# Optimization experiments

Hardware: AMD Instinct MI355X
Metric: run time of the kernel (lower is better)

The kernel has to match this reference:

```python
import jax, jax.numpy as jnp
import numpy as np

N = 1_000_000   # mesh points
D_IN = 5        # scalar invariants
H = 128         # hidden width
L = 5           # hidden layers
NB = 10         # tensor bases

# t0 generator basis rows (flattened 3x3 deviatoric diag tensors)
T01 = np.array([-1/3, 0, 0, 0, 1/6, 0, 0, 0, 1/6], dtype=np.float32)
T02 = np.array([1/6, 0, 0, 0, -1/3, 0, 0, 0, 1/6], dtype=np.float32)
T03 = np.array([1/6, 0, 0, 0, 1/6, 0, 0, 0, -1/3], dtype=np.float32)


def _linear_params(k, fan_in, fan_out):
    # xavier_uniform_ with gain=1.0, bias filled with 0.01 (as in init_w_and_b)
    limit = float(np.sqrt(6.0 / (fan_in + fan_out)))
    W = jax.random.uniform(k, (fan_in, fan_out), jnp.float32, -limit, limit)
    b = jnp.full((fan_out,), 0.01, jnp.float32)
    return W, b


def setup_inputs() -> dict:
    key = jax.random.key(0)
    ks = jax.random.split(key, 16)
    x = jax.random.normal(ks[0], (N, D_IN), jnp.float32)
    tb = jax.random.normal(ks[1], (N, NB, 9), jnp.float32)
    inp = {"x": x, "tb": tb}
    dims = [D_IN] + [H] * L
    for i in range(L):
        W, b = _linear_params(ks[2 + i], dims[i], dims[i + 1])
        inp[f"W{i+1}"] = W
        inp[f"b{i+1}"] = b
    inp["Wc"], inp["bc"] = _linear_params(ks[2 + L], H, NB)
    inp["Wg1"], inp["bg1"] = _linear_params(ks[3 + L], H, 1)
    inp["Wg2"], inp["bg2"] = _linear_params(ks[4 + L], H, 1)
    inp["Wg3"], inp["bg3"] = _linear_params(ks[5 + L], H, 1)
    return inp


def reference(x, tb, W1, b1, W2, b2, W3, b3, W4, b4, W5, b5,
              Wc, bc, Wg1, bg1, Wg2, bg2, Wg3, bg3):
    h = x
    for W, b in ((W1, b1), (W2, b2), (W3, b3), (W4, b4), (W5, b5)):
        h = jax.nn.relu(h @ W + b)          # [N, H]
    coeffs = h @ Wc + bc                     # [N, NB]
    g1 = h @ Wg1 + bg1                       # [N, 1]
    g2 = h @ Wg2 + bg2
    g3 = h @ Wg3 + bg3
    t0 = g1 * jnp.asarray(T01) + g2 * jnp.asarray(T02) + g3 * jnp.asarray(T03)  # [N, 9]
    # batched tensor-basis contraction replacing the per-point double loop
    bij = t0 + jnp.einsum('nt,ntc->nc', coeffs, tb)  # [N, 9]
    return bij
```

## Files before the change

kernel.cpp:

```cpp
#include <hip/hip_runtime.h>
#include <stdint.h>


#define NPTS   1000000
#define TPB    512
#define NBLKS  256
#define PTILE  512
#define NT     ((NPTS + PTILE - 1) / PTILE)

typedef uint32_t u32;
typedef __attribute__((ext_vector_type(4)))  u32   u32x4;
typedef __attribute__((ext_vector_type(8)))  short s16x8;
typedef __attribute__((ext_vector_type(16))) float f32x16;
typedef __attribute__((ext_vector_type(4), aligned(4))) float f32x4u;

#define WS_L(l)   ((l)*65536)
#define WS_TAIL   262144
#define WS_W1     (262144 + 8192)
#define WS_BIAS   (262144 + 12288)

#define LDS_BUF0   0
#define LDS_BUF1   65536
#define LDS_HEADS  131072
#define LDS_W1     (131072 + 8192)
#define LDS_BIAS   (131072 + 12288)
#define LDS_TOTAL  147456

#define MFMA(a,b,c) __builtin_amdgcn_mfma_f32_32x32x16_bf16((a),(b),(c),0,0,0)
#define BC16(v)     __builtin_bit_cast(s16x8, (v))

__device__ __forceinline__ u32 cvtpk(float lo, float hi) {
    u32 r;
    asm("v_cvt_pk_bf16_f32 %0, %1, %2" : "=v"(r) : "v"(lo), "v"(hi));
    return r;
}
__device__ __forceinline__ float lo2f(u32 p){ return __builtin_bit_cast(float, p << 16); }
__device__ __forceinline__ float hi2f(u32 p){ return __builtin_bit_cast(float, p & 0xffff0000u); }
__device__ __forceinline__ uint16_t f2bf(float f) {
    u32 u = __builtin_bit_cast(u32, f);
    return (uint16_t)((u + 0x7fffu + ((u >> 16) & 1u)) >> 16);
}
__device__ __forceinline__ float b2f(uint16_t h){ return __builtin_bit_cast(float, (u32)h << 16); }

__device__ __forceinline__ void stageN(const char* g, char* l, int tid, int nbytes) {
    const int w = tid >> 6, ln = tid & 63;
    const char* gp = g + w*1024 + ln*16;
    char* lp = l + w*1024;
    #pragma unroll
    for (int i = 0; i < 8; ++i) {
        if (i*8192 >= nbytes) break;
        __builtin_amdgcn_global_load_lds(
            (const __attribute__((address_space(1))) uint32_t*)(gp + i*8192),
            (__attribute__((address_space(3))) uint32_t*)(lp + i*8192), 16, 0, 0);
    }
}

extern "C" __global__ void __launch_bounds__(256)
tbnn_prep(const float* __restrict__ W1, const float* __restrict__ b1,
          const float* __restrict__ W2, const float* __restrict__ b2,
          const float* __restrict__ W3, const float* __restrict__ b3,
          const float* __restrict__ W4, const float* __restrict__ b4,
          const float* __restrict__ W5, const float* __restrict__ b5,
          const float* __restrict__ Wc, const float* __restrict__ bc,
          const float* __restrict__ Wg1,const float* __restrict__ bg1,
          const float* __restrict__ Wg2,const float* __restrict__ bg2,
          const float* __restrict__ Wg3,const float* __restrict__ bg3,
          char* __restrict__ ws)
{
    int idx = blockIdx.x*256 + threadIdx.x;
    if (idx < 65536) {
        int l = idx >> 14, r = idx & 16383, ifc = r >> 7, of = r & 127;
        const float* Wt = (l==0)?W2:(l==1)?W3:(l==2)?W4:W5;
        float w = Wt[ifc*128 + of];
        uint16_t hb = f2bf(w);
        uint16_t lb = f2bf(w - b2f(hb));
        char* row = ws + WS_L(l) + of*512;
        int o = (2*ifc) ^ ((of&15)<<4);
        *(uint16_t*)(row + o)       = hb;
        *(uint16_t*)(row + 256 + o) = lb;
    } else if (idx < 65536 + 2048) {
        int j = idx - 65536, of = j >> 7, ifc = j & 127;
        float v = 0.f;
        if      (of < 10)  v = Wc[ifc*10 + of];
        else if (of == 10) v = Wg1[ifc];
        else if (of == 11) v = Wg2[ifc];
        else if (of == 12) v = Wg3[ifc];
        uint16_t hb = f2bf(v);
        uint16_t lb = f2bf(v - b2f(hb));
        char* row = ws + WS_TAIL + of*512;
        int o = (2*ifc) ^ ((of&15)<<4);
        *(uint16_t*)(row + o)       = hb;
        *(uint16_t*)(row + 256 + o) = lb;
    } else if (idx < 65536 + 2048 + 128) {
        int of = idx - (65536 + 2048);
        uint16_t* dst = (uint16_t*)(ws + WS_W1 + of*32);
        #pragma unroll
        for (int s = 0; s < 5; ++s) {
            float w = W1[s*128 + of];
            uint16_t hb = f2bf(w);
            dst[s]      = hb;
            dst[6 + s]  = f2bf(w - b2f(hb));
            dst[11 + s] = hb;
        }
        dst[5] = f2bf(b1[of]);
    } else if (idx < 65536 + 2048 + 128 + 544) {
        int j = idx - (65536 + 2048 + 128);
        float v = 0.f;
        if (j < 512) {
            int l = j >> 7, of = j & 127;
            const float* bt = (l==0)?b2:(l==1)?b3:(l==2)?b4:b5;
            v = bt[of];
        } else {
            int of = j - 512;
            if      (of < 10)  v = bc[of];
            else if (of == 10) v = bg1[0];
            else if (of == 11) v = bg2[0];
            else if (of == 12) v = bg3[0];
        }
        *(uint16_t*)(ws + WS_BIAS + j*2) = f2bf(v);
    }
}

extern "C" __global__ void __launch_bounds__(TPB)
tbnn_main(const float* __restrict__ x, const float* __restrict__ tb,
          const char* __restrict__ ws, float* __restrict__ out)
{
    extern __shared__ char smem[];
    const int tid  = threadIdx.x;
    const int wave = tid >> 6;
    const int lane = tid & 63;
    const int col  = lane & 31;
    const int hi   = lane >> 5;
    const int sm   = (col & 15) << 4;
    const int hib  = hi * 16;

    stageN(ws + WS_TAIL, smem + LDS_HEADS, tid, 16384);
    stageN(ws + WS_L(0), smem + LDS_BUF0,  tid, 65536);
    stageN(ws + WS_L(1), smem + LDS_BUF1,  tid, 65536);
    __syncthreads();

    u32x4 Bc; Bc[0] = hi ? 0u : 0x00003F80u; Bc[1]=0u; Bc[2]=0u; Bc[3]=0u;
    f32x16 zf;
    #pragma unroll
    for (int i = 0; i < 16; ++i) zf[i] = 0.f;

    f32x16 acc[4];
    u32x4  B1h[8], B1l[8], B2h[8], B2l[8];

    auto convert = [&](u32x4* BH, u32x4* BL) {
        #pragma unroll
        for (int ot = 0; ot < 4; ++ot) {
            f32x16 a = acc[ot];
            #pragma unroll
            for (int h2 = 0; h2 < 2; ++h2) {
                float e0 = fmaxf(a[8*h2+0], 0.f), e1 = fmaxf(a[8*h2+1], 0.f);
                float e2 = fmaxf(a[8*h2+2], 0.f), e3 = fmaxf(a[8*h2+3], 0.f);
                float e4 = fmaxf(a[8*h2+4], 0.f), e5 = fmaxf(a[8*h2+5], 0.f);
                float e6 = fmaxf(a[8*h2+6], 0.f), e7 = fmaxf(a[8*h2+7], 0.f);
                u32 h01 = cvtpk(e0,e1), h23 = cvtpk(e2,e3);
                u32 h45 = cvtpk(e4,e5), h67 = cvtpk(e6,e7);
                u32 l01 = cvtpk(e0 - lo2f(h01), e1 - hi2f(h01));
                u32 l23 = cvtpk(e2 - lo2f(h23), e3 - hi2f(h23));
                u32 l45 = cvtpk(e4 - lo2f(h45), e5 - hi2f(h45));
                u32 l67 = cvtpk(e6 - lo2f(h67), e7 - hi2f(h67));
                auto sh1 = __builtin_amdgcn_permlane32_swap(h01, h45, false, false);
                auto sh2 = __builtin_amdgcn_permlane32_swap(h23, h67, false, false);
                u32x4 fh; fh[0]=sh1[0]; fh[1]=sh2[0]; fh[2]=sh1[1]; fh[3]=sh2[1];
                BH[2*ot+h2] = fh;
                auto sl1 = __builtin_amdgcn_permlane32_swap(l01, l45, false, false);
                auto sl2 = __builtin_amdgcn_permlane32_swap(l23, l67, false, false);
                u32x4 fl; fl[0]=sl1[0]; fl[1]=sl2[0]; fl[2]=sl1[1]; fl[3]=sl2[1];
                BL[2*ot+h2] = fl;
            }
        }
    };

    auto l1 = [&](int p) {
        float x0=0.f,x1=0.f,x2=0.f,x3=0.f,x4=0.f;
        if (p < NPTS) {
            const float* xp = x + (size_t)p*5;
            f32x4u v = *(const f32x4u*)xp;
            x0=v.x; x1=v.y; x2=v.z; x3=v.w; x4=xp[4];
        }
        float h0 = lo2f(cvtpk(x0,x0)), l0 = x0 - h0;
        float h1 = lo2f(cvtpk(x1,x1)), l1v = x1 - h1;
        float h2 = lo2f(cvtpk(x2,x2)), l2 = x2 - h2;
        float h3 = lo2f(cvtpk(x3,x3)), l3 = x3 - h3;
        float h4 = lo2f(cvtpk(x4,x4)), l4 = x4 - h4;
        u32x4 Bx;
        if (hi == 0) {
            Bx[0] = cvtpk(h0,h1); Bx[1] = cvtpk(h2,h3);
            Bx[2] = cvtpk(h4,1.0f); Bx[3] = cvtpk(h0,h1);
        } else {
            Bx[0] = cvtpk(h2,h3); Bx[1] = cvtpk(h4,l0);
            Bx[2] = cvtpk(l1v,l2); Bx[3] = cvtpk(l3,l4);
        }
        #pragma unroll
        for (int ot = 0; ot < 4; ++ot) {
            u32x4 Av = *(const u32x4*)(smem + LDS_W1 + (ot*32+col)*32 + hib);
            acc[ot] = MFMA(BC16(Av), BC16(Bx), zf);
        }
    };

    auto kloop = [&](const char* wb, const u32x4* BH, const u32x4* BL) {
        #pragma unroll
        for (int k = 0; k < 8; ++k) {
            int so = (k*32 + hib) ^ sm;
            const char* rp = wb + col*512 + so;
            u32x4 H0 = *(const u32x4*)(rp);
            u32x4 L0v = *(const u32x4*)(rp + 256);
            u32x4 H1 = *(const u32x4*)(rp + 32*512);
            u32x4 L1v = *(const u32x4*)(rp + 32*512 + 256);
            u32x4 H2 = *(const u32x4*)(rp + 64*512);
            u32x4 L2v = *(const u32x4*)(rp + 64*512 + 256);
            u32x4 H3 = *(const u32x4*)(rp + 96*512);
            u32x4 L3v = *(const u32x4*)(rp + 96*512 + 256);
            s16x8 bl = BC16(BL[k]), bh = BC16(BH[k]);
            acc[0] = MFMA(BC16(H0), bl, (k==0)?zf:acc[0]);
            acc[1] = MFMA(BC16(H1), bl, (k==0)?zf:acc[1]);
            acc[2] = MFMA(BC16(H2), bl, (k==0)?zf:acc[2]);
            acc[3] = MFMA(BC16(H3), bl, (k==0)?zf:acc[3]);
            acc[0] = MFMA(BC16(H0), bh, acc[0]);
            acc[1] = MFMA(BC16(H1), bh, acc[1]);
            acc[2] = MFMA(BC16(H2), bh, acc[2]);
            acc[3] = MFMA(BC16(H3), bh, acc[3]);
            acc[0] = MFMA(BC16(L0v), bh, acc[0]);
            acc[1] = MFMA(BC16(L1v), bh, acc[1]);
            acc[2] = MFMA(BC16(L2v), bh, acc[2]);
            acc[3] = MFMA(BC16(L3v), bh, acc[3]);
        }
    };
    auto biask = [&](int lc) {
        #pragma unroll
        for (int ot = 0; ot < 4; ++ot) {
            u32 bw = (u32)*(const uint16_t*)(smem + LDS_BIAS + (lc*128 + ot*32 + col)*2);
            u32x4 Ab; Ab[0] = hi ? 0u : bw; Ab[1]=0u; Ab[2]=0u; Ab[3]=0u;
            acc[ot] = MFMA(BC16(Ab), BC16(Bc), acc[ot]);
        }
    };

    auto headsg = [&](const u32x4* BH, const u32x4* BL) -> f32x16 {
        f32x16 h6;
        #pragma unroll
        for (int k = 0; k < 8; ++k) {
            int so = (k*32 + hib) ^ sm;
            const char* rp = smem + LDS_HEADS + (col&15)*512;
            u32x4 HH = *(const u32x4*)(rp + so);
            u32x4 HL = *(const u32x4*)(rp + 256 + so);
            h6 = MFMA(BC16(HH), BC16(BL[k]), (k==0)?zf:h6);
            h6 = MFMA(BC16(HH), BC16(BH[k]), h6);
            h6 = MFMA(BC16(HL), BC16(BH[k]), h6);
        }
        u32 bw = (u32)*(const uint16_t*)(smem + LDS_BIAS + (512 + col)*2);
        u32x4 Ab; Ab[0] = hi ? 0u : bw; Ab[1]=0u; Ab[2]=0u; Ab[3]=0u;
        return MFMA(BC16(Ab), BC16(Bc), h6);
    };

    auto contraction = [&](int p, f32x16 c) {
        if (p >= NPTS) return;
        const float* tbp = tb + (size_t)p*90;
        const float sixth = 0.16666666666666666f;
        const float third = 0.3333333333333333f;
        float s[9];
        if (hi == 0) {
            float g1 = c[6], g2 = c[7];
            s[0] = -g1*third + g2*sixth;
            s[4] =  g1*sixth - g2*third;
            s[8] =  g1*sixth + g2*sixth;
        } else {
            float g3 = c[4];
            s[0] =  g3*sixth;
            s[4] =  g3*sixth;
            s[8] = -g3*third;
        }
        s[1]=s[2]=s[3]=s[5]=s[6]=s[7]=0.f;
        #pragma unroll
        for (int j = 0; j < 4; ++j) {
            int trow = (hi ? 4 : 0) + j;
            float cf = c[j];
            const float* r = tbp + trow*9;
            f32x4u r0 = *(const f32x4u*)(r);
            f32x4u r1 = *(const f32x4u*)(r + 4);
            float r8 = r[8];
            s[0] += cf*r0.x; s[1] += cf*r0.y; s[2] += cf*r0.z; s[3] += cf*r0.w;
            s[4] += cf*r1.x; s[5] += cf*r1.y; s[6] += cf*r1.z; s[7] += cf*r1.w;
            s[8] += cf*r8;
        }
        if (hi == 0) {
            #pragma unroll
            for (int j = 4; j < 6; ++j) {
                int trow = 4 + j;
                float cf = c[j];
                const float* r = tbp + trow*9;
                f32x4u r0 = *(const f32x4u*)(r);
                f32x4u r1 = *(const f32x4u*)(r + 4);
                float r8 = r[8];
                s[0] += cf*r0.x; s[1] += cf*r0.y; s[2] += cf*r0.z; s[3] += cf*r0.w;
                s[4] += cf*r1.x; s[5] += cf*r1.y; s[6] += cf*r1.z; s[7] += cf*r1.w;
                s[8] += cf*r8;
            }
        }
        #pragma unroll
        for (int j = 0; j < 9; ++j) {
            u32 uv = __builtin_bit_cast(u32, s[j]);
            auto rr = __builtin_amdgcn_permlane32_swap(uv, uv, false, false);
            s[j] = __builtin_bit_cast(float, (u32)rr[0]) + __builtin_bit_cast(float, (u32)rr[1]);
        }
        if (hi == 0) {
            float* op = out + (size_t)p*9;
            f32x4u o0, o1;
            o0.x=s[0]; o0.y=s[1]; o0.z=s[2]; o0.w=s[3];
            o1.x=s[4]; o1.y=s[5]; o1.z=s[6]; o1.w=s[7];
            *(f32x4u*)op       = o0;
            *(f32x4u*)(op + 4) = o1;
            op[8] = s[8];
        }
    };

    for (int t = blockIdx.x; t < NT; t += gridDim.x) {
        const int p1 = t*PTILE + wave*64 + col;
        const int p2 = p1 + 32;

        l1(p1); convert(B1h, B1l);
        l1(p2); convert(B2h, B2l);
        __syncthreads();

        __builtin_amdgcn_s_setprio(1); kloop(smem + LDS_BUF0, B1h, B1l); biask(0); __builtin_amdgcn_s_setprio(0);
        convert(B1h, B1l);
        __builtin_amdgcn_s_setprio(1); kloop(smem + LDS_BUF0, B2h, B2l); biask(0); __builtin_amdgcn_s_setprio(0);
        convert(B2h, B2l);
        __syncthreads();
        stageN(ws + WS_L(2), smem + LDS_BUF0, tid, 65536);

        __builtin_amdgcn_s_setprio(1); kloop(smem + LDS_BUF1, B1h, B1l); biask(1); __builtin_amdgcn_s_setprio(0);
        convert(B1h, B1l);
        __builtin_amdgcn_s_setprio(1); kloop(smem + LDS_BUF1, B2h, B2l); biask(1); __builtin_amdgcn_s_setprio(0);
        convert(B2h, B2l);
        __syncthreads();
        stageN(ws + WS_L(3), smem + LDS_BUF1, tid, 65536);

        __builtin_amdgcn_s_setprio(1); kloop(smem + LDS_BUF0, B1h, B1l); biask(2); __builtin_amdgcn_s_setprio(0);
        convert(B1h, B1l);
        __builtin_amdgcn_s_setprio(1); kloop(smem + LDS_BUF0, B2h, B2l); biask(2); __builtin_amdgcn_s_setprio(0);
        convert(B2h, B2l);
        __syncthreads();
        stageN(ws + WS_L(0), smem + LDS_BUF0, tid, 65536);

        __builtin_amdgcn_s_setprio(1); kloop(smem + LDS_BUF1, B1h, B1l); biask(3); __builtin_amdgcn_s_setprio(0);
        convert(B1h, B1l);
        __builtin_amdgcn_s_setprio(1); kloop(smem + LDS_BUF1, B2h, B2l); biask(3); __builtin_amdgcn_s_setprio(0);
        convert(B2h, B2l);
        __syncthreads();
        stageN(ws + WS_L(1), smem + LDS_BUF1, tid, 65536);

        __builtin_amdgcn_s_setprio(1);
        f32x16 h6a = headsg(B1h, B1l);
        __builtin_amdgcn_s_setprio(0);
        contraction(p1, h6a);
        __builtin_amdgcn_s_setprio(1);
        f32x16 h6b = headsg(B2h, B2l);
        __builtin_amdgcn_s_setprio(0);
        contraction(p2, h6b);
    }
    __syncthreads();
}

extern "C" void kernel_launch(void* const* d_in, const int* in_sizes, int n_in,
                              void* d_out, int out_size, void* d_ws, size_t ws_size,
                              hipStream_t stream) {
    (void)in_sizes; (void)n_in; (void)out_size; (void)ws_size;
    char* ws = (char*)d_ws;
    hipLaunchKernelGGL(tbnn_prep, dim3(267), dim3(256), 0, stream,
        (const float*)d_in[2],  (const float*)d_in[3],
        (const float*)d_in[4],  (const float*)d_in[5],
        (const float*)d_in[6],  (const float*)d_in[7],
        (const float*)d_in[8],  (const float*)d_in[9],
        (const float*)d_in[10], (const float*)d_in[11],
        (const float*)d_in[12], (const float*)d_in[13],
        (const float*)d_in[14], (const float*)d_in[15],
        (const float*)d_in[16], (const float*)d_in[17],
        (const float*)d_in[18], (const float*)d_in[19],
        ws);
    (void)hipFuncSetAttribute((const void*)tbnn_main,
                              hipFuncAttributeMaxDynamicSharedMemorySize, LDS_TOTAL);
    hipLaunchKernelGGL(tbnn_main, dim3(NBLKS), dim3(TPB), LDS_TOTAL, stream,
        (const float*)d_in[0], (const float*)d_in[1], ws, (float*)d_out);
}
```

Baseline: 479.1 us.

## Halve block to 4 waves each processing four 32-point groups

Cuts the main kernel to 256 threads per block, so each wave now handles 128 points (four groups of 32) instead of 64. Activations for all four groups stay in registers, which doubles the per-wave reuse of each LDS weight tile and halves the number of waves reading LDS. The staging loop is adjusted so four waves still cover the full weight buffers, and the s_setprio hints are removed. The cost is much higher register pressure (launch bounds set to one block) and fewer waves to hide latency.

```diff
diff --git a/kernel.cpp b/kernel.cpp
--- a/kernel.cpp
+++ b/kernel.cpp
@@ -3,7 +3,7 @@
 
 
 #define NPTS   1000000
-#define TPB    512
+#define TPB    256
 #define NBLKS  256
 #define PTILE  512
 #define NT     ((NPTS + PTILE - 1) / PTILE)
@@ -47,11 +47,11 @@
     const char* gp = g + w*1024 + ln*16;
     char* lp = l + w*1024;
     #pragma unroll
-    for (int i = 0; i < 8; ++i) {
-        if (i*8192 >= nbytes) break;
+    for (int i = 0; i < 16; ++i) {
+        if (i*4096 >= nbytes) break;
         __builtin_amdgcn_global_load_lds(
-            (const __attribute__((address_space(1))) uint32_t*)(gp + i*8192),
-            (__attribute__((address_space(3))) uint32_t*)(lp + i*8192), 16, 0, 0);
+            (const __attribute__((address_space(1))) uint32_t*)(gp + i*4096),
+            (__attribute__((address_space(3))) uint32_t*)(lp + i*4096), 16, 0, 0);
     }
 }
 
@@ -121,7 +121,7 @@
     }
 }
 
-extern "C" __global__ void __launch_bounds__(TPB)
+extern "C" __global__ void __launch_bounds__(TPB, 1)
 tbnn_main(const float* __restrict__ x, const float* __restrict__ tb,
           const char* __restrict__ ws, float* __restrict__ out)
 {
@@ -145,9 +145,9 @@
     for (int i = 0; i < 16; ++i) zf[i] = 0.f;
 
     f32x16 acc[4];
-    u32x4  B1h[8], B1l[8], B2h[8], B2l[8];
-
-    auto convert = [&](u32x4* BH, u32x4* BL) {
+    u32x4  Bh[4][8], Bl[4][8];
+
+    auto convert = [&](u32x4 (&BH)[8], u32x4 (&BL)[8]) {
         #pragma unroll
         for (int ot = 0; ot < 4; ++ot) {
             f32x16 a = acc[ot];
@@ -202,7 +202,7 @@
         }
     };
 
-    auto kloop = [&](const char* wb, const u32x4* BH, const u32x4* BL) {
+    auto kloop = [&](const char* wb, const u32x4 (&BH)[8], const u32x4 (&BL)[8]) {
         #pragma unroll
         for (int k = 0; k < 8; ++k) {
             int so = (k*32 + hib) ^ sm;
@@ -239,7 +239,7 @@
         }
     };
 
-    auto headsg = [&](const u32x4* BH, const u32x4* BL) -> f32x16 {
+    auto headsg = [&](const u32x4 (&BH)[8], const u32x4 (&BL)[8]) -> f32x16 {
         f32x16 h6;
         #pragma unroll
         for (int k = 0; k < 8; ++k) {
@@ -318,49 +318,37 @@
     };
 
     for (int t = blockIdx.x; t < NT; t += gridDim.x) {
-        const int p1 = t*PTILE + wave*64 + col;
-        const int p2 = p1 + 32;
-
-        l1(p1); convert(B1h, B1l);
-        l1(p2); convert(B2h, B2l);
-        __syncthreads();
-
-        __builtin_amdgcn_s_setprio(1); kloop(smem + LDS_BUF0, B1h, B1l); biask(0); __builtin_amdgcn_s_setprio(0);
-        convert(B1h, B1l);
-        __builtin_amdgcn_s_setprio(1); kloop(smem + LDS_BUF0, B2h, B2l); biask(0); __builtin_amdgcn_s_setprio(0);
-        convert(B2h, B2l);
+        const int pb = t*PTILE + wave*128;
+
+        #pragma unroll
+        for (int g = 0; g < 4; ++g) { l1(pb + g*32 + col); convert(Bh[g], Bl[g]); }
+        __syncthreads();
+
+        #pragma unroll
+        for (int g = 0; g < 4; ++g) { kloop(smem + LDS_BUF0, Bh[g], Bl[g]); biask(0); convert(Bh[g], Bl[g]); }
         __syncthreads();
         stageN(ws + WS_L(2), smem + LDS_BUF0, tid, 65536);
 
-        __builtin_amdgcn_s_setprio(1); kloop(smem + LDS_BUF1, B1h, B1l); biask(1); __builtin_amdgcn_s_setprio(0);
-        convert(B1h, B1l);
-        __builtin_amdgcn_s_setprio(1); kloop(smem + LDS_BUF1, B2h, B2l); biask(1); __builtin_amdgcn_s_setprio(0);
-        convert(B2h, B2l);
+        #pragma unroll
+        for (int g = 0; g < 4; ++g) { kloop(smem + LDS_BUF1, Bh[g], Bl[g]); biask(1); convert(Bh[g], Bl[g]); }
         __syncthreads();
         stageN(ws + WS_L(3), smem + LDS_BUF1, tid, 65536);
 
-        __builtin_amdgcn_s_setprio(1); kloop(smem + LDS_BUF0, B1h, B1l); biask(2); __builtin_amdgcn_s_setprio(0);
-        convert(B1h, B1l);
-        __builtin_amdgcn_s_setprio(1); kloop(smem + LDS_BUF0, B2h, B2l); biask(2); __builtin_amdgcn_s_setprio(0);
-        convert(B2h, B2l);
+        #pragma unroll
+        for (int g = 0; g < 4; ++g) { kloop(smem + LDS_BUF0, Bh[g], Bl[g]); biask(2); convert(Bh[g], Bl[g]); }
         __syncthreads();
         stageN(ws + WS_L(0), smem + LDS_BUF0, tid, 65536);
 
-        __builtin_amdgcn_s_setprio(1); kloop(smem + LDS_BUF1, B1h, B1l); biask(3); __builtin_amdgcn_s_setprio(0);
-        convert(B1h, B1l);
-        __builtin_amdgcn_s_setprio(1); kloop(smem + LDS_BUF1, B2h, B2l); biask(3); __builtin_amdgcn_s_setprio(0);
-        convert(B2h, B2l);
+        #pragma unroll
+        for (int g = 0; g < 4; ++g) { kloop(smem + LDS_BUF1, Bh[g], Bl[g]); biask(3); convert(Bh[g], Bl[g]); }
         __syncthreads();
         stageN(ws + WS_L(1), smem + LDS_BUF1, tid, 65536);
 
-        __builtin_amdgcn_s_setprio(1);
-        f32x16 h6a = headsg(B1h, B1l);
-        __builtin_amdgcn_s_setprio(0);
-        contraction(p1, h6a);
-        __builtin_amdgcn_s_setprio(1);
-        f32x16 h6b = headsg(B2h, B2l);
-        __builtin_amdgcn_s_setprio(0);
-        contraction(p2, h6b);
+        #pragma unroll
+        for (int g = 0; g < 4; ++g) {
+            f32x16 h6 = headsg(Bh[g], Bl[g]);
+            contraction(pb + g*32 + col, h6);
+        }
     }
     __syncthreads();
 }
```

Result: slower. 1.096 ms (+128.7%).
